# Optimization experiments

Hardware: AMD Instinct MI355X
Metric: run time of the kernel (lower is better)

Reference implementation:

```python
import jax, jax.numpy as jnp
import numpy as np

N = 100000
E_ADJ = 800000
E_RAY = 800000
IN_DIM = 2
HID = 64
HEADS = 2
NEG_SLOPE = 0.2  # PyG GATv2Conv default


def setup_inputs() -> dict:
    key = jax.random.key(0)
    ks = jax.random.split(key, 16)
    s = 0.1
    p = lambda k, shape: (jax.random.normal(k, shape, jnp.float32) * s)
    inp = {
        "x": jax.random.normal(ks[0], (N, IN_DIM), jnp.float32),
        "edge_adj": jax.random.randint(ks[1], (2, E_ADJ), 0, N, jnp.int32),
        "edge_ray": jax.random.randint(ks[2], (2, E_RAY), 0, N, jnp.int32),
        # layer 1 params, stacked over the 2 relation types [adjacent, ray]
        "l1_Wl": p(ks[3], (2, IN_DIM, HEADS * HID)),
        "l1_bl": jnp.zeros((2, HEADS * HID), jnp.float32),
        "l1_Wr": p(ks[4], (2, IN_DIM, HEADS * HID)),
        "l1_br": jnp.zeros((2, HEADS * HID), jnp.float32),
        "l1_att": p(ks[5], (2, HEADS, HID)),
        "l1_bias": jnp.zeros((2, HID), jnp.float32),
        # layer 2 params
        "l2_Wl": p(ks[6], (2, HID, HEADS * HID)),
        "l2_bl": jnp.zeros((2, HEADS * HID), jnp.float32),
        "l2_Wr": p(ks[7], (2, HID, HEADS * HID)),
        "l2_br": jnp.zeros((2, HEADS * HID), jnp.float32),
        "l2_att": p(ks[8], (2, HEADS, HID)),
        "l2_bias": jnp.zeros((2, HID), jnp.float32),
    }
    return inp


def _gatv2(x, src, dst, Wl, bl, Wr, br, att, bias):
    # GATv2Conv, concat=False, add_self_loops=False (PyG semantics)
    n = x.shape[0]
    H, C = att.shape
    xl = (x @ Wl + bl).reshape(n, H, C)  # source transform
    xr = (x @ Wr + br).reshape(n, H, C)  # target transform
    e = jax.nn.leaky_relu(xl[src] + xr[dst], NEG_SLOPE)  # [E,H,C]
    score = jnp.einsum('ehc,hc->eh', e, att)             # [E,H]
    # segment softmax over incoming edges per destination (per head)
    m = jax.ops.segment_max(score, dst, num_segments=n)  # only gathered at non-empty segs
    ex = jnp.exp(score - m[dst])
    denom = jax.ops.segment_sum(ex, dst, num_segments=n)
    alpha = ex / (denom[dst] + 1e-16)                    # [E,H]
    out = jax.ops.segment_sum(xl[src] * alpha[:, :, None], dst, num_segments=n)  # [N,H,C]
    return out.mean(axis=1) + bias                       # concat=False -> head mean


def _hetero_layer(x, ea, er, Wl, bl, Wr, br, att, bias):
    o_adj = _gatv2(x, ea[0], ea[1], Wl[0], bl[0], Wr[0], br[0], att[0], bias[0])
    o_ray = _gatv2(x, er[0], er[1], Wl[1], bl[1], Wr[1], br[1], att[1], bias[1])
    return 0.5 * (o_adj + o_ray)  # HeteroConv aggr='mean' over 2 relations


def reference(x, edge_adj, edge_ray,
              l1_Wl, l1_bl, l1_Wr, l1_br, l1_att, l1_bias,
              l2_Wl, l2_bl, l2_Wr, l2_br, l2_att, l2_bias):
    h = _hetero_layer(x, edge_adj, edge_ray, l1_Wl, l1_bl, l1_Wr, l1_br, l1_att, l1_bias)
    h = jax.nn.relu(h)
    out = _hetero_layer(h, edge_adj, edge_ray, l2_Wl, l2_bl, l2_Wr, l2_br, l2_att, l2_bias)
    return out
```

## Files before the change

kernel.cpp:

```cpp
#include <hip/hip_runtime.h>
#include <hip/hip_bf16.h>

typedef __hip_bfloat16 bf16;
typedef unsigned int uint;
typedef unsigned short ushort;
typedef __attribute__((ext_vector_type(8))) short short8;
typedef __attribute__((ext_vector_type(4))) float floatx4;

#define N_NODES 100000
#define N_PAD   100096
#define E_EDGES 800000
#define NBLK    98
#define EBLK    3125

static __device__ __forceinline__ uint packbf(float a, float b) {
  bf16 x = __float2bfloat16(a), y = __float2bfloat16(b);
  ushort ux = *reinterpret_cast<ushort*>(&x);
  ushort uy = *reinterpret_cast<ushort*>(&y);
  return (uint)ux | ((uint)uy << 16);
}
static __device__ __forceinline__ float lo16(uint u) { return __uint_as_float(u << 16); }
static __device__ __forceinline__ float hi16(uint u) { return __uint_as_float(u & 0xffff0000u); }

__global__ __launch_bounds__(256) void rank_k(
    const int* __restrict__ dst0, const int* __restrict__ dst1,
    int* fi0, int* fi1, int* __restrict__ rk0, int* __restrict__ rk1) {
  int i = blockIdx.x * 256 + threadIdx.x;
  int rel = blockIdx.y;
  const int* dst = rel ? dst1 : dst0;
  int* fi = rel ? fi1 : fi0;
  int* rk = rel ? rk1 : rk0;
  int d = dst[i];
  rk[i] = atomicAdd(&fi[d], 1);
}

__global__ __launch_bounds__(256) void scat_rank_k(
    const int* __restrict__ src0, const int* __restrict__ dst0,
    const int* __restrict__ src1, const int* __restrict__ dst1,
    const int* __restrict__ rk0, const int* __restrict__ rk1,
    const int* __restrict__ rp0, const int* __restrict__ rp1,
    int2* __restrict__ csd0, int2* __restrict__ csd1) {
  int i = blockIdx.x * 256 + threadIdx.x;
  int rel = blockIdx.y;
  const int* src = rel ? src1 : src0;
  const int* dst = rel ? dst1 : dst0;
  const int* rk = rel ? rk1 : rk0;
  const int* rp = rel ? rp1 : rp0;
  int2* csd = rel ? csd1 : csd0;
  int d = dst[i];
  int s = src[i];
  int pos = rp[d] + rk[i];
  csd[pos] = make_int2(s, d);
}

__global__ void scan_blk_k(const int* __restrict__ deg0, const int* __restrict__ deg1,
                           int* rp0, int* rp1, int* bsum) {
  __shared__ int s[1024];
  int r = blockIdx.y;
  const int* deg = r ? deg1 : deg0;
  int* rp = r ? rp1 : rp0;
  int i = blockIdx.x * 1024 + threadIdx.x;
  int v = (i < N_NODES) ? deg[i] : 0;
  s[threadIdx.x] = v;
  __syncthreads();
  for (int off = 1; off < 1024; off <<= 1) {
    int t = (threadIdx.x >= off) ? s[threadIdx.x - off] : 0;
    __syncthreads();
    s[threadIdx.x] += t;
    __syncthreads();
  }
  if (i < N_NODES) rp[i] = s[threadIdx.x] - v;
  if (threadIdx.x == 1023) bsum[r * NBLK + blockIdx.x] = s[1023];
}

__global__ void scan_top_k(int* bsum, int* rp0, int* rp1) {
  __shared__ int s[128];
  int r = blockIdx.x;
  int v = (threadIdx.x < NBLK) ? bsum[r * NBLK + threadIdx.x] : 0;
  s[threadIdx.x] = v;
  __syncthreads();
  for (int off = 1; off < 128; off <<= 1) {
    int t = (threadIdx.x >= off) ? s[threadIdx.x - off] : 0;
    __syncthreads();
    s[threadIdx.x] += t;
    __syncthreads();
  }
  if (threadIdx.x < NBLK) bsum[r * NBLK + threadIdx.x] = s[threadIdx.x] - v;
  if (threadIdx.x == 127) (r ? rp1 : rp0)[N_NODES] = s[127];
}

__global__ void scan_add_k(const int* __restrict__ bsum,
                           int* rp0, int* rp1, int* fi0, int* fi1) {
  int r = blockIdx.y;
  int i = blockIdx.x * 1024 + threadIdx.x;
  if (i >= N_NODES) return;
  int* rp = r ? rp1 : rp0;
  int* fi = r ? fi1 : fi0;
  int val = rp[i] + bsum[r * NBLK + blockIdx.x];
  rp[i] = val;
  fi[i] = val;
}

__global__ void wprep_k(const float* __restrict__ Wl, const float* __restrict__ Wr,
                        short* __restrict__ WT,
                        const float* __restrict__ l1Wl, const float* __restrict__ l1bl,
                        const float* __restrict__ l1Wr, const float* __restrict__ l1br,
                        const float* __restrict__ l1att, float* __restrict__ L1C) {
  if (blockIdx.x == 128) {
    int t = threadIdx.x;
    if (t < 20) {
      int rel = t / 10, rem = t % 10, h = rem / 5, v = rem % 5;
      const float* a = l1att + rel * 128 + h * 64;
      float sum = 0.f;
      for (int c = 0; c < 64; ++c) {
        int cc = h * 64 + c;
        float val;
        if (v == 0)      val = l1bl[rel * 128 + cc] + l1br[rel * 128 + cc];
        else if (v == 1) val = l1Wr[rel * 256 + cc];
        else if (v == 2) val = l1Wr[rel * 256 + 128 + cc];
        else if (v == 3) val = l1Wl[rel * 256 + cc];
        else             val = l1Wl[rel * 256 + 128 + cc];
        sum += a[c] * val;
      }
      L1C[t] = sum;
    }
    return;
  }
  int id2 = blockIdx.x * 256 + threadIdx.x;
  int rel = id2 >> 14;
  int id = id2 & 16383;
  int c = id >> 6, k = id & 63;
  const float* W = (c < 128) ? (Wl + rel * 8192) : (Wr + rel * 8192);
  int cc = c & 127;
  bf16 b = __float2bfloat16(W[k * 128 + cc]);
  WT[rel * 16384 + c * 64 + k] = *reinterpret_cast<short*>(&b);
}

__global__ __launch_bounds__(256) void l1score_k(
    const int2* __restrict__ csd0, const int2* __restrict__ csd1,
    const float* __restrict__ x,
    const float* __restrict__ Wl, const float* __restrict__ bl,
    const float* __restrict__ Wr, const float* __restrict__ br,
    const float* __restrict__ att, const float* __restrict__ l1c,
    float4* __restrict__ EX4) {
  __shared__ float sC[32 * 24];
  int rel = blockIdx.y;
  const int2* csd = rel ? csd1 : csd0;
  const float* Wl_r = Wl + rel * 256;
  const float* Wr_r = Wr + rel * 256;
  const float* bl_r = bl + rel * 128;
  const float* br_r = br + rel * 128;
  const float* att_r = att + rel * 128;
  int t = threadIdx.x;
  if (t < 128) {
    int c = t, ch = c >> 2, o = c & 3;
    sC[ch * 24 + 0 + o]  = bl_r[c] + br_r[c];
    sC[ch * 24 + 4 + o]  = Wr_r[c];
    sC[ch * 24 + 8 + o]  = Wr_r[128 + c];
    sC[ch * 24 + 12 + o] = Wl_r[c];
    sC[ch * 24 + 16 + o] = Wl_r[128 + c];
    sC[ch * 24 + 20 + o] = att_r[c];
  }
  const float* C = l1c + rel * 10;
  float q00 = C[0], qv00 = C[1], qv10 = C[2], qw00 = C[3], qw10 = C[4];
  float q01 = C[5], qv01 = C[6], qv11 = C[7], qw01 = C[8], qw11 = C[9];
  __syncthreads();
  int i = blockIdx.x * 256 + t;
  int2 sd = csd[i];
  int s = sd.x, d = sd.y;
  float2 xs = *(const float2*)(x + 2 * s);
  float2 xd = *(const float2*)(x + 2 * d);
  float t0a = 0.f, t0b = 0.f, t1a = 0.f, t1b = 0.f;
#pragma unroll
  for (int ch = 0; ch < 32; ++ch) {
    const float4* cp = (const float4*)(sC + ch * 24);
    float4 bb = cp[0], v0 = cp[1], v1 = cp[2], w0 = cp[3], w1 = cp[4], aa = cp[5];
    float e0 = bb.x + xd.x * v0.x + xd.y * v1.x + xs.x * w0.x + xs.y * w1.x;
    float e1 = bb.y + xd.x * v0.y + xd.y * v1.y + xs.x * w0.y + xs.y * w1.y;
    float e2 = bb.z + xd.x * v0.z + xd.y * v1.z + xs.x * w0.z + xs.y * w1.z;
    float e3 = bb.w + xd.x * v0.w + xd.y * v1.w + xs.x * w0.w + xs.y * w1.w;
    if (ch < 16) {
      t0a = fmaf(aa.x, fabsf(e0), t0a); t0b = fmaf(aa.y, fabsf(e1), t0b);
      t0a = fmaf(aa.z, fabsf(e2), t0a); t0b = fmaf(aa.w, fabsf(e3), t0b);
    } else {
      t1a = fmaf(aa.x, fabsf(e0), t1a); t1b = fmaf(aa.y, fabsf(e1), t1b);
      t1a = fmaf(aa.z, fabsf(e2), t1a); t1b = fmaf(aa.w, fabsf(e3), t1b);
    }
  }
  float T0 = t0a + t0b, T1 = t1a + t1b;
  float lin0 = q00 + xd.x * qv00 + xd.y * qv10 + xs.x * qw00 + xs.y * qw10;
  float lin1 = q01 + xd.x * qv01 + xd.y * qv11 + xs.x * qw01 + xs.y * qw11;
  float p0 = fmaf(0.4f, T0, 0.6f * lin0);
  float p1 = fmaf(0.4f, T1, 0.6f * lin1);
  EX4[(size_t)rel * E_EDGES + i] = make_float4(__expf(p0), __expf(p1), xs.x, xs.y);
}

__global__ __launch_bounds__(256) void l1agg_k(
    const int* __restrict__ rp0, const int* __restrict__ rp1,
    const float4* __restrict__ EX4, float* __restrict__ NA) {
  int g = (blockIdx.x * 256 + threadIdx.x) >> 2;
  int k = threadIdx.x & 3;
  if (g >= N_NODES) return;
  float p0 = 0.f, p1 = 0.f, p2 = 0.f, p3 = 0.f, p4 = 0.f, p5 = 0.f;
  float p6 = 0.f, p7 = 0.f, p8 = 0.f, p9 = 0.f, p10 = 0.f, p11 = 0.f;
  {
    int beg = rp0[g], end = rp0[g + 1];
    for (int j = beg + k; j < end; j += 4) {
      float4 e = EX4[j];
      p0 += e.x; p1 = fmaf(e.x, e.z, p1); p2 = fmaf(e.x, e.w, p2);
      p3 += e.y; p4 = fmaf(e.y, e.z, p4); p5 = fmaf(e.y, e.w, p5);
    }
  }
  {
    const float4* E1 = EX4 + E_EDGES;
    int beg = rp1[g], end = rp1[g + 1];
    for (int j = beg + k; j < end; j += 4) {
      float4 e = E1[j];
      p6 += e.x; p7 = fmaf(e.x, e.z, p7); p8 = fmaf(e.x, e.w, p8);
      p9 += e.y; p10 = fmaf(e.y, e.z, p10); p11 = fmaf(e.y, e.w, p11);
    }
  }
#define RED4(v) v += __shfl_xor(v, 1); v += __shfl_xor(v, 2);
  RED4(p0) RED4(p1) RED4(p2) RED4(p3) RED4(p4) RED4(p5)
  RED4(p6) RED4(p7) RED4(p8) RED4(p9) RED4(p10) RED4(p11)
#undef RED4
  float* na = NA + (size_t)g * 16;
  if (k == 0)      *(float4*)(na)     = make_float4(p0, p1, p2, p3);
  else if (k == 1) *(float4*)(na + 4) = make_float4(p4, p5, p6, p7);
  else if (k == 2) *(float4*)(na + 8) = make_float4(p8, p9, p10, p11);
}

__global__ __launch_bounds__(256) void l1finish_k(
    const float* __restrict__ NA,
    const float* __restrict__ Wl, const float* __restrict__ bl,
    const float* __restrict__ bias, uint2* __restrict__ HB2) {
  int idx = blockIdx.x * 256 + threadIdx.x;
  int d = idx >> 4, l = idx & 15;
  int c0 = 4 * l;
  const float* na = NA + (size_t)d * 16;
  float out0 = 0.f, out1 = 0.f, out2 = 0.f, out3 = 0.f;
#pragma unroll
  for (int r = 0; r < 2; ++r) {
    float a0c = 0.f, a1c = 0.f, a2c = 0.f, a3c = 0.f;
#pragma unroll
    for (int h = 0; h < 2; ++h) {
      float den = na[r * 6 + h * 3 + 0];
      float A0  = na[r * 6 + h * 3 + 1];
      float A1  = na[r * 6 + h * 3 + 2];
      float inv = 1.f / (den + 1e-16f);
      float a0 = A0 * inv, a1 = A1 * inv, S = den * inv;
      float4 W0 = *(const float4*)(Wl + r * 256 + h * 64 + c0);
      float4 W1 = *(const float4*)(Wl + r * 256 + 128 + h * 64 + c0);
      float4 B  = *(const float4*)(bl + r * 128 + h * 64 + c0);
      a0c += a0 * W0.x + a1 * W1.x + S * B.x;
      a1c += a0 * W0.y + a1 * W1.y + S * B.y;
      a2c += a0 * W0.z + a1 * W1.z + S * B.z;
      a3c += a0 * W0.w + a1 * W1.w + S * B.w;
    }
    float4 bi = *(const float4*)(bias + r * 64 + c0);
    out0 += 0.5f * a0c + bi.x;
    out1 += 0.5f * a1c + bi.y;
    out2 += 0.5f * a2c + bi.z;
    out3 += 0.5f * a3c + bi.w;
  }
  out0 = fmaxf(0.5f * out0, 0.f); out1 = fmaxf(0.5f * out1, 0.f);
  out2 = fmaxf(0.5f * out2, 0.f); out3 = fmaxf(0.5f * out3, 0.f);
  HB2[(size_t)d * 16 + l] = make_uint2(packbf(out0, out1), packbf(out2, out3));
}

__global__ __launch_bounds__(256) void mfma_t_k(const bf16* __restrict__ HB,
                                                const short* __restrict__ WTb,
                                                const float* __restrict__ blb,
                                                const float* __restrict__ brb,
                                                bf16* __restrict__ XL0,
                                                bf16* __restrict__ XR0,
                                                bf16* __restrict__ XL1,
                                                bf16* __restrict__ XR1) {
  __shared__ short sW[256 * 72];
  int rel = blockIdx.z;
  const short* WT = WTb + rel * 16384;
  const float* bl = blb + rel * 128;
  const float* br = brb + rel * 128;
  bf16* XLp = rel ? XL1 : XL0;
  bf16* XRp = rel ? XR1 : XR0;
  int t = threadIdx.x;
#pragma unroll
  for (int i = 0; i < 8; ++i) {
    int chunk = t + i * 256;
    int c = chunk >> 3, off = (chunk & 7) * 8;
    *(short8*)(&sW[c * 72 + off]) = *(const short8*)(WT + chunk * 8);
  }
  __syncthreads();
  int wave = t >> 6, lane = t & 63;
  int q = lane >> 4, m = lane & 15;
  int rowbase = blockIdx.x * 128 + wave * 32;
  short8 afr[2][2];
#pragma unroll
  for (int rt = 0; rt < 2; ++rt)
#pragma unroll
    for (int kh = 0; kh < 2; ++kh) {
      size_t row = (size_t)(rowbase + rt * 16 + m);
      afr[rt][kh] = *(const short8*)((const short*)HB + row * 64 + kh * 32 + q * 8);
    }
  for (int ct = 0; ct < 16; ++ct) {
    int col = ct * 16 + m;
    short8 b0 = *(const short8*)(&sW[col * 72 + q * 8]);
    short8 b1 = *(const short8*)(&sW[col * 72 + 32 + q * 8]);
    float bias = (col < 128) ? bl[col] : br[col - 128];
    bf16* X = (col < 128) ? XLp : XRp;
    int c128 = col & 127;
#pragma unroll
    for (int rt = 0; rt < 2; ++rt) {
      floatx4 acc = {0.f, 0.f, 0.f, 0.f};
      acc = __builtin_amdgcn_mfma_f32_16x16x32_bf16(afr[rt][0], b0, acc, 0, 0, 0);
      acc = __builtin_amdgcn_mfma_f32_16x16x32_bf16(afr[rt][1], b1, acc, 0, 0, 0);
      int r0 = rowbase + rt * 16 + q * 4;
#pragma unroll
      for (int i2 = 0; i2 < 4; ++i2) {
        int row = r0 + i2;
        if (row < N_NODES)
          X[(size_t)row * 128 + c128] = __float2bfloat16(acc[i2] + bias);
      }
    }
  }
}

struct EdgeAcc { float a0, a1, a2, a3, den; };

static __device__ __forceinline__ void edge_step(
    uint2 u, float xr0, float xr1, float xr2, float xr3,
    float at0, float at1, float at2, float at3, EdgeAcc& A) {
  float x0 = lo16(u.x), x1 = hi16(u.x), x2 = lo16(u.y), x3 = hi16(u.y);
  float e0 = x0 + xr0; e0 = e0 > 0.f ? e0 : 0.2f * e0;
  float e1 = x1 + xr1; e1 = e1 > 0.f ? e1 : 0.2f * e1;
  float e2 = x2 + xr2; e2 = e2 > 0.f ? e2 : 0.2f * e2;
  float e3 = x3 + xr3; e3 = e3 > 0.f ? e3 : 0.2f * e3;
  float p = e0 * at0 + e1 * at1 + e2 * at2 + e3 * at3;
  p += __shfl_xor(p, 1);
  p += __shfl_xor(p, 2);
  p += __shfl_xor(p, 4);
  p += __shfl_xor(p, 8);
  float ex = __expf(p);
  A.den += ex;
  A.a0 += ex * x0; A.a1 += ex * x1; A.a2 += ex * x2; A.a3 += ex * x3;
}

__global__ __launch_bounds__(256) void aggf_k(
    const int* __restrict__ rp0, const int2* __restrict__ csd0,
    const int* __restrict__ rp1, const int2* __restrict__ csd1,
    const bf16* __restrict__ XL0, const bf16* __restrict__ XR0,
    const bf16* __restrict__ XL1, const bf16* __restrict__ XR1,
    const float* __restrict__ att,
    const float* __restrict__ bias,
    float* __restrict__ outf) {
  int d = (blockIdx.x * 256 + threadIdx.x) >> 6;
  int lane = threadIdx.x & 63;
  if (d >= N_NODES) return;
  int half = lane >> 5;
  int l = lane & 31;
  int beg0 = rp0[d], end0 = rp0[d + 1];
  int beg1 = rp1[d], end1 = rp1[d + 1];
  const float* at = att + 4 * l;
  const float* bt = att + 128 + 4 * l;
  float at0 = at[0], at1 = at[1], at2 = at[2], at3 = at[3];
  float bt0 = bt[0], bt1 = bt[1], bt2 = bt[2], bt3 = bt[3];
  uint2 ur0 = *(const uint2*)(XR0 + (size_t)d * 128 + 4 * l);
  uint2 ur1 = *(const uint2*)(XR1 + (size_t)d * 128 + 4 * l);
  float xa0 = lo16(ur0.x), xa1 = hi16(ur0.x), xa2 = lo16(ur0.y), xa3 = hi16(ur0.y);
  float xb0 = lo16(ur1.x), xb1 = hi16(ur1.x), xb2 = lo16(ur1.y), xb3 = hi16(ur1.y);
  EdgeAcc A = {0.f, 0.f, 0.f, 0.f, 0.f};
  EdgeAcc B = {0.f, 0.f, 0.f, 0.f, 0.f};
  {
    int j = beg0 + half;
    for (; j + 2 < end0; j += 4) {
      int sA = csd0[j].x, sB = csd0[j + 2].x;
      uint2 uA = *(const uint2*)(XL0 + (size_t)sA * 128 + 4 * l);
      uint2 uB = *(const uint2*)(XL0 + (size_t)sB * 128 + 4 * l);
      edge_step(uA, xa0, xa1, xa2, xa3, at0, at1, at2, at3, A);
      edge_step(uB, xa0, xa1, xa2, xa3, at0, at1, at2, at3, A);
    }
    for (; j < end0; j += 2) {
      int s = csd0[j].x;
      uint2 u = *(const uint2*)(XL0 + (size_t)s * 128 + 4 * l);
      edge_step(u, xa0, xa1, xa2, xa3, at0, at1, at2, at3, A);
    }
  }
  {
    int j = beg1 + half;
    for (; j + 2 < end1; j += 4) {
      int sA = csd1[j].x, sB = csd1[j + 2].x;
      uint2 uA = *(const uint2*)(XL1 + (size_t)sA * 128 + 4 * l);
      uint2 uB = *(const uint2*)(XL1 + (size_t)sB * 128 + 4 * l);
      edge_step(uA, xb0, xb1, xb2, xb3, bt0, bt1, bt2, bt3, B);
      edge_step(uB, xb0, xb1, xb2, xb3, bt0, bt1, bt2, bt3, B);
    }
    for (; j < end1; j += 2) {
      int s = csd1[j].x;
      uint2 u = *(const uint2*)(XL1 + (size_t)s * 128 + 4 * l);
      edge_step(u, xb0, xb1, xb2, xb3, bt0, bt1, bt2, bt3, B);
    }
  }
#define C32(v) v += __shfl_xor(v, 32);
  C32(A.den) C32(A.a0) C32(A.a1) C32(A.a2) C32(A.a3)
  C32(B.den) C32(B.a0) C32(B.a1) C32(B.a2) C32(B.a3)
#undef C32
  float invA = 1.f / (A.den + 1e-16f);
  float invB = 1.f / (B.den + 1e-16f);
  A.a0 *= invA; A.a1 *= invA; A.a2 *= invA; A.a3 *= invA;
  B.a0 *= invB; B.a1 *= invB; B.a2 *= invB; B.a3 *= invB;
  float t0 = 0.5f * (A.a0 + __shfl_xor(A.a0, 16));
  float t1 = 0.5f * (A.a1 + __shfl_xor(A.a1, 16));
  float t2 = 0.5f * (A.a2 + __shfl_xor(A.a2, 16));
  float t3 = 0.5f * (A.a3 + __shfl_xor(A.a3, 16));
  float u0 = 0.5f * (B.a0 + __shfl_xor(B.a0, 16));
  float u1 = 0.5f * (B.a1 + __shfl_xor(B.a1, 16));
  float u2 = 0.5f * (B.a2 + __shfl_xor(B.a2, 16));
  float u3 = 0.5f * (B.a3 + __shfl_xor(B.a3, 16));
  if (lane >= 16) return;
  int c0 = 4 * lane;
  t0 += bias[c0]; t1 += bias[c0 + 1]; t2 += bias[c0 + 2]; t3 += bias[c0 + 3];
  u0 += bias[64 + c0]; u1 += bias[64 + c0 + 1];
  u2 += bias[64 + c0 + 2]; u3 += bias[64 + c0 + 3];
  float v0 = 0.5f * (t0 + u0);
  float v1 = 0.5f * (t1 + u1);
  float v2 = 0.5f * (t2 + u2);
  float v3 = 0.5f * (t3 + u3);
  *(float4*)(outf + (size_t)d * 64 + c0) = make_float4(v0, v1, v2, v3);
}

extern "C" void kernel_launch(void* const* d_in, const int* in_sizes, int n_in,
                              void* d_out, int out_size, void* d_ws, size_t ws_size,
                              hipStream_t stream) {
  const float* x       = (const float*)d_in[0];
  const int*   e_adj   = (const int*)d_in[1];
  const int*   e_ray   = (const int*)d_in[2];
  const float* l1_Wl   = (const float*)d_in[3];
  const float* l1_bl   = (const float*)d_in[4];
  const float* l1_Wr   = (const float*)d_in[5];
  const float* l1_br   = (const float*)d_in[6];
  const float* l1_att  = (const float*)d_in[7];
  const float* l1_bias = (const float*)d_in[8];
  const float* l2_Wl   = (const float*)d_in[9];
  const float* l2_bl   = (const float*)d_in[10];
  const float* l2_Wr   = (const float*)d_in[11];
  const float* l2_br   = (const float*)d_in[12];
  const float* l2_att  = (const float*)d_in[13];
  const float* l2_bias = (const float*)d_in[14];
  float* out = (float*)d_out;

  char* w = (char*)d_ws;
  size_t off = 0;
  auto alloc = [&](size_t bytes) -> char* {
    char* p = w + off;
    off += (bytes + 255) & ~(size_t)255;
    return p;
  };
  bf16* XL0  = (bf16*)alloc((size_t)N_PAD * 128 * 2);
  bf16* XR0  = (bf16*)alloc((size_t)N_PAD * 128 * 2);
  bf16* XL1  = (bf16*)alloc((size_t)N_PAD * 128 * 2);
  bf16* XR1  = (bf16*)alloc((size_t)N_PAD * 128 * 2);
  bf16* HB   = (bf16*)alloc((size_t)N_PAD * 64 * 2);
  short* WT  = (short*)alloc(2 * 16384 * 2);
  int* RP0   = (int*)alloc((size_t)(N_NODES + 1) * 4);
  int* RP1   = (int*)alloc((size_t)(N_NODES + 1) * 4);
  int* FI0   = (int*)alloc((size_t)N_NODES * 4);
  int* FI1   = (int*)alloc((size_t)N_NODES * 4);
  int2* CSD0 = (int2*)alloc((size_t)E_EDGES * 8);
  int2* CSD1 = (int2*)alloc((size_t)E_EDGES * 8);
  int* BSUM  = (int*)alloc(2 * NBLK * 4);
  float* L1C = (float*)alloc(20 * 4);

  float4* EX4 = (float4*)XL0;
  float* NA   = (float*)((char*)XL0 + 25600000);
  int* RK0    = (int*)XL1;
  int* RK1    = (int*)((char*)XL1 + 3200000);

  const int* src_adj = e_adj;
  const int* dst_adj = e_adj + E_EDGES;
  const int* src_ray = e_ray;
  const int* dst_ray = e_ray + E_EDGES;

  const int WNB = (N_NODES * 64) / 256;
  const int MB  = N_PAD / 128;

  size_t fispan = (size_t)((char*)FI1 - (char*)FI0) + (size_t)N_NODES * 4;
  hipMemsetAsync(FI0, 0, fispan, stream);
  rank_k<<<dim3(EBLK, 2), 256, 0, stream>>>(dst_adj, dst_ray, FI0, FI1, RK0, RK1);
  scan_blk_k<<<dim3(NBLK, 2), 1024, 0, stream>>>(FI0, FI1, RP0, RP1, BSUM);
  scan_top_k<<<2, 128, 0, stream>>>(BSUM, RP0, RP1);
  scan_add_k<<<dim3(NBLK, 2), 1024, 0, stream>>>(BSUM, RP0, RP1, FI0, FI1);
  scat_rank_k<<<dim3(EBLK, 2), 256, 0, stream>>>(src_adj, dst_adj, src_ray, dst_ray,
                                                 RK0, RK1, RP0, RP1, CSD0, CSD1);
  wprep_k<<<129, 256, 0, stream>>>(l2_Wl, l2_Wr, WT,
                                   l1_Wl, l1_bl, l1_Wr, l1_br, l1_att, L1C);

  l1score_k<<<dim3(EBLK, 2), 256, 0, stream>>>(
      CSD0, CSD1, x, l1_Wl, l1_bl, l1_Wr, l1_br, l1_att, L1C, EX4);
  l1agg_k<<<(N_NODES * 4 + 255) / 256, 256, 0, stream>>>(RP0, RP1, EX4, NA);
  l1finish_k<<<(N_NODES * 16) / 256, 256, 0, stream>>>(NA, l1_Wl, l1_bl, l1_bias,
                                                       (uint2*)HB);

  mfma_t_k<<<dim3(MB, 1, 2), 256, 0, stream>>>(HB, WT, l2_bl, l2_br,
                                               XL0, XR0, XL1, XR1);
  aggf_k<<<WNB, 256, 0, stream>>>(RP0, CSD0, RP1, CSD1, XL0, XR0, XL1, XR1,
                                  l2_att, l2_bias, out);
}
```

Before: 423.3 us.

## Widen layer-2 edge gathers to 16-byte loads and precompute layer-1 coefficient table

The final aggregation kernel now splits each wavefront into four groups of 16 lanes. Each lane loads 8 bf16 features with one 16-byte load instead of 4 with an 8-byte load, so four edges are processed in parallel per wave instead of two, and the per-edge shuffle reduction drops one step. The layer-1 score kernel no longer rebuilds its coefficient table in shared memory with a block barrier. It reads a table that the weight-prep kernel writes once to global memory. The trade-offs are more registers per lane and more cross-group reduction shuffles at the end. The score kernel's table reads now go through the global/constant cache instead of LDS.

```diff
diff --git a/kernel.cpp b/kernel.cpp
--- a/kernel.cpp
+++ b/kernel.cpp
@@ -105,9 +105,21 @@
                         short* __restrict__ WT,
                         const float* __restrict__ l1Wl, const float* __restrict__ l1bl,
                         const float* __restrict__ l1Wr, const float* __restrict__ l1br,
-                        const float* __restrict__ l1att, float* __restrict__ L1C) {
+                        const float* __restrict__ l1att, float* __restrict__ L1C,
+                        float* __restrict__ SCG) {
   if (blockIdx.x == 128) {
     int t = threadIdx.x;
+    {
+      int rel = t >> 7, c = t & 127;
+      int ch = c >> 2, o = c & 3;
+      float* g = SCG + rel * 768 + ch * 24;
+      g[0 + o]  = l1bl[rel * 128 + c] + l1br[rel * 128 + c];
+      g[4 + o]  = l1Wr[rel * 256 + c];
+      g[8 + o]  = l1Wr[rel * 256 + 128 + c];
+      g[12 + o] = l1Wl[rel * 256 + c];
+      g[16 + o] = l1Wl[rel * 256 + 128 + c];
+      g[20 + o] = l1att[rel * 128 + c];
+    }
     if (t < 20) {
       int rel = t / 10, rem = t % 10, h = rem / 5, v = rem % 5;
       const float* a = l1att + rel * 128 + h * 64;
@@ -139,33 +151,15 @@
 __global__ __launch_bounds__(256) void l1score_k(
     const int2* __restrict__ csd0, const int2* __restrict__ csd1,
     const float* __restrict__ x,
-    const float* __restrict__ Wl, const float* __restrict__ bl,
-    const float* __restrict__ Wr, const float* __restrict__ br,
-    const float* __restrict__ att, const float* __restrict__ l1c,
+    const float* __restrict__ scg, const float* __restrict__ l1c,
     float4* __restrict__ EX4) {
-  __shared__ float sC[32 * 24];
   int rel = blockIdx.y;
   const int2* csd = rel ? csd1 : csd0;
-  const float* Wl_r = Wl + rel * 256;
-  const float* Wr_r = Wr + rel * 256;
-  const float* bl_r = bl + rel * 128;
-  const float* br_r = br + rel * 128;
-  const float* att_r = att + rel * 128;
-  int t = threadIdx.x;
-  if (t < 128) {
-    int c = t, ch = c >> 2, o = c & 3;
-    sC[ch * 24 + 0 + o]  = bl_r[c] + br_r[c];
-    sC[ch * 24 + 4 + o]  = Wr_r[c];
-    sC[ch * 24 + 8 + o]  = Wr_r[128 + c];
-    sC[ch * 24 + 12 + o] = Wl_r[c];
-    sC[ch * 24 + 16 + o] = Wl_r[128 + c];
-    sC[ch * 24 + 20 + o] = att_r[c];
-  }
+  const float* sC = scg + rel * 768;
   const float* C = l1c + rel * 10;
   float q00 = C[0], qv00 = C[1], qv10 = C[2], qw00 = C[3], qw10 = C[4];
   float q01 = C[5], qv01 = C[6], qv11 = C[7], qw01 = C[8], qw11 = C[9];
-  __syncthreads();
-  int i = blockIdx.x * 256 + t;
+  int i = blockIdx.x * 256 + threadIdx.x;
   int2 sd = csd[i];
   int s = sd.x, d = sd.y;
   float2 xs = *(const float2*)(x + 2 * s);
@@ -325,24 +319,28 @@
   }
 }
 
-struct EdgeAcc { float a0, a1, a2, a3, den; };
-
-static __device__ __forceinline__ void edge_step(
-    uint2 u, float xr0, float xr1, float xr2, float xr3,
-    float at0, float at1, float at2, float at3, EdgeAcc& A) {
-  float x0 = lo16(u.x), x1 = hi16(u.x), x2 = lo16(u.y), x3 = hi16(u.y);
-  float e0 = x0 + xr0; e0 = e0 > 0.f ? e0 : 0.2f * e0;
-  float e1 = x1 + xr1; e1 = e1 > 0.f ? e1 : 0.2f * e1;
-  float e2 = x2 + xr2; e2 = e2 > 0.f ? e2 : 0.2f * e2;
-  float e3 = x3 + xr3; e3 = e3 > 0.f ? e3 : 0.2f * e3;
-  float p = e0 * at0 + e1 * at1 + e2 * at2 + e3 * at3;
+static __device__ __forceinline__ void edge_step16(
+    uint4 u, const float (&xr)[8], const float (&at)[8],
+    float (&a)[8], float& den) {
+  float x[8];
+  x[0] = lo16(u.x); x[1] = hi16(u.x);
+  x[2] = lo16(u.y); x[3] = hi16(u.y);
+  x[4] = lo16(u.z); x[5] = hi16(u.z);
+  x[6] = lo16(u.w); x[7] = hi16(u.w);
+  float p = 0.f;
+#pragma unroll
+  for (int j = 0; j < 8; ++j) {
+    float e = x[j] + xr[j];
+    float le = fmaxf(e, 0.2f * e);
+    p = fmaf(at[j], le, p);
+  }
   p += __shfl_xor(p, 1);
   p += __shfl_xor(p, 2);
   p += __shfl_xor(p, 4);
-  p += __shfl_xor(p, 8);
   float ex = __expf(p);
-  A.den += ex;
-  A.a0 += ex * x0; A.a1 += ex * x1; A.a2 += ex * x2; A.a3 += ex * x3;
+  den += ex;
+#pragma unroll
+  for (int j = 0; j < 8; ++j) a[j] = fmaf(ex, x[j], a[j]);
 }
 
 __global__ __launch_bounds__(256) void aggf_k(
@@ -356,76 +354,99 @@
   int d = (blockIdx.x * 256 + threadIdx.x) >> 6;
   int lane = threadIdx.x & 63;
   if (d >= N_NODES) return;
-  int half = lane >> 5;
-  int l = lane & 31;
+  int g = lane >> 4;
+  int k = lane & 15;
   int beg0 = rp0[d], end0 = rp0[d + 1];
   int beg1 = rp1[d], end1 = rp1[d + 1];
-  const float* at = att + 4 * l;
-  const float* bt = att + 128 + 4 * l;
-  float at0 = at[0], at1 = at[1], at2 = at[2], at3 = at[3];
-  float bt0 = bt[0], bt1 = bt[1], bt2 = bt[2], bt3 = bt[3];
-  uint2 ur0 = *(const uint2*)(XR0 + (size_t)d * 128 + 4 * l);
-  uint2 ur1 = *(const uint2*)(XR1 + (size_t)d * 128 + 4 * l);
-  float xa0 = lo16(ur0.x), xa1 = hi16(ur0.x), xa2 = lo16(ur0.y), xa3 = hi16(ur0.y);
-  float xb0 = lo16(ur1.x), xb1 = hi16(ur1.x), xb2 = lo16(ur1.y), xb3 = hi16(ur1.y);
-  EdgeAcc A = {0.f, 0.f, 0.f, 0.f, 0.f};
-  EdgeAcc B = {0.f, 0.f, 0.f, 0.f, 0.f};
+  float at0[8], at1[8], xr0v[8], xr1v[8];
   {
-    int j = beg0 + half;
-    for (; j + 2 < end0; j += 4) {
-      int sA = csd0[j].x, sB = csd0[j + 2].x;
-      uint2 uA = *(const uint2*)(XL0 + (size_t)sA * 128 + 4 * l);
-      uint2 uB = *(const uint2*)(XL0 + (size_t)sB * 128 + 4 * l);
-      edge_step(uA, xa0, xa1, xa2, xa3, at0, at1, at2, at3, A);
-      edge_step(uB, xa0, xa1, xa2, xa3, at0, at1, at2, at3, A);
-    }
-    for (; j < end0; j += 2) {
+    float4 a0 = *(const float4*)(att + 8 * k);
+    float4 a1 = *(const float4*)(att + 8 * k + 4);
+    at0[0] = a0.x; at0[1] = a0.y; at0[2] = a0.z; at0[3] = a0.w;
+    at0[4] = a1.x; at0[5] = a1.y; at0[6] = a1.z; at0[7] = a1.w;
+    float4 b0 = *(const float4*)(att + 128 + 8 * k);
+    float4 b1 = *(const float4*)(att + 128 + 8 * k + 4);
+    at1[0] = b0.x; at1[1] = b0.y; at1[2] = b0.z; at1[3] = b0.w;
+    at1[4] = b1.x; at1[5] = b1.y; at1[6] = b1.z; at1[7] = b1.w;
+    uint4 uA = *(const uint4*)((const char*)XR0 + (size_t)d * 256 + k * 16);
+    xr0v[0] = lo16(uA.x); xr0v[1] = hi16(uA.x);
+    xr0v[2] = lo16(uA.y); xr0v[3] = hi16(uA.y);
+    xr0v[4] = lo16(uA.z); xr0v[5] = hi16(uA.z);
+    xr0v[6] = lo16(uA.w); xr0v[7] = hi16(uA.w);
+    uint4 uB = *(const uint4*)((const char*)XR1 + (size_t)d * 256 + k * 16);
+    xr1v[0] = lo16(uB.x); xr1v[1] = hi16(uB.x);
+    xr1v[2] = lo16(uB.y); xr1v[3] = hi16(uB.y);
+    xr1v[4] = lo16(uB.z); xr1v[5] = hi16(uB.z);
+    xr1v[6] = lo16(uB.w); xr1v[7] = hi16(uB.w);
+  }
+  float aA[8] = {0.f, 0.f, 0.f, 0.f, 0.f, 0.f, 0.f, 0.f};
+  float aB[8] = {0.f, 0.f, 0.f, 0.f, 0.f, 0.f, 0.f, 0.f};
+  float denA = 0.f, denB = 0.f;
+  {
+    int j = beg0 + g;
+    for (; j + 4 < end0; j += 8) {
+      int sA = csd0[j].x, sB = csd0[j + 4].x;
+      uint4 uA = *(const uint4*)((const char*)XL0 + (size_t)sA * 256 + k * 16);
+      uint4 uB = *(const uint4*)((const char*)XL0 + (size_t)sB * 256 + k * 16);
+      edge_step16(uA, xr0v, at0, aA, denA);
+      edge_step16(uB, xr0v, at0, aA, denA);
+    }
+    for (; j < end0; j += 4) {
       int s = csd0[j].x;
-      uint2 u = *(const uint2*)(XL0 + (size_t)s * 128 + 4 * l);
-      edge_step(u, xa0, xa1, xa2, xa3, at0, at1, at2, at3, A);
+      uint4 u = *(const uint4*)((const char*)XL0 + (size_t)s * 256 + k * 16);
+      edge_step16(u, xr0v, at0, aA, denA);
     }
   }
   {
-    int j = beg1 + half;
-    for (; j + 2 < end1; j += 4) {
-      int sA = csd1[j].x, sB = csd1[j + 2].x;
-      uint2 uA = *(const uint2*)(XL1 + (size_t)sA * 128 + 4 * l);
-      uint2 uB = *(const uint2*)(XL1 + (size_t)sB * 128 + 4 * l);
-      edge_step(uA, xb0, xb1, xb2, xb3, bt0, bt1, bt2, bt3, B);
-      edge_step(uB, xb0, xb1, xb2, xb3, bt0, bt1, bt2, bt3, B);
-    }
-    for (; j < end1; j += 2) {
+    int j = beg1 + g;
+    for (; j + 4 < end1; j += 8) {
+      int sA = csd1[j].x, sB = csd1[j + 4].x;
+      uint4 uA = *(const uint4*)((const char*)XL1 + (size_t)sA * 256 + k * 16);
+      uint4 uB = *(const uint4*)((const char*)XL1 + (size_t)sB * 256 + k * 16);
+      edge_step16(uA, xr1v, at1, aB, denB);
+      edge_step16(uB, xr1v, at1, aB, denB);
+    }
+    for (; j < end1; j += 4) {
       int s = csd1[j].x;
-      uint2 u = *(const uint2*)(XL1 + (size_t)s * 128 + 4 * l);
-      edge_step(u, xb0, xb1, xb2, xb3, bt0, bt1, bt2, bt3, B);
-    }
-  }
-#define C32(v) v += __shfl_xor(v, 32);
-  C32(A.den) C32(A.a0) C32(A.a1) C32(A.a2) C32(A.a3)
-  C32(B.den) C32(B.a0) C32(B.a1) C32(B.a2) C32(B.a3)
-#undef C32
-  float invA = 1.f / (A.den + 1e-16f);
-  float invB = 1.f / (B.den + 1e-16f);
-  A.a0 *= invA; A.a1 *= invA; A.a2 *= invA; A.a3 *= invA;
-  B.a0 *= invB; B.a1 *= invB; B.a2 *= invB; B.a3 *= invB;
-  float t0 = 0.5f * (A.a0 + __shfl_xor(A.a0, 16));
-  float t1 = 0.5f * (A.a1 + __shfl_xor(A.a1, 16));
-  float t2 = 0.5f * (A.a2 + __shfl_xor(A.a2, 16));
-  float t3 = 0.5f * (A.a3 + __shfl_xor(A.a3, 16));
-  float u0 = 0.5f * (B.a0 + __shfl_xor(B.a0, 16));
-  float u1 = 0.5f * (B.a1 + __shfl_xor(B.a1, 16));
-  float u2 = 0.5f * (B.a2 + __shfl_xor(B.a2, 16));
-  float u3 = 0.5f * (B.a3 + __shfl_xor(B.a3, 16));
-  if (lane >= 16) return;
-  int c0 = 4 * lane;
-  t0 += bias[c0]; t1 += bias[c0 + 1]; t2 += bias[c0 + 2]; t3 += bias[c0 + 3];
-  u0 += bias[64 + c0]; u1 += bias[64 + c0 + 1];
-  u2 += bias[64 + c0 + 2]; u3 += bias[64 + c0 + 3];
-  float v0 = 0.5f * (t0 + u0);
-  float v1 = 0.5f * (t1 + u1);
-  float v2 = 0.5f * (t2 + u2);
-  float v3 = 0.5f * (t3 + u3);
-  *(float4*)(outf + (size_t)d * 64 + c0) = make_float4(v0, v1, v2, v3);
+      uint4 u = *(const uint4*)((const char*)XL1 + (size_t)s * 256 + k * 16);
+      edge_step16(u, xr1v, at1, aB, denB);
+    }
+  }
+#pragma unroll
+  for (int j = 0; j < 8; ++j) {
+    aA[j] += __shfl_xor(aA[j], 16); aA[j] += __shfl_xor(aA[j], 32);
+    aB[j] += __shfl_xor(aB[j], 16); aB[j] += __shfl_xor(aB[j], 32);
+  }
+  denA += __shfl_xor(denA, 16); denA += __shfl_xor(denA, 32);
+  denB += __shfl_xor(denB, 16); denB += __shfl_xor(denB, 32);
+  float invA = 1.f / (denA + 1e-16f);
+  float invB = 1.f / (denB + 1e-16f);
+  float tA[8], tB[8];
+#pragma unroll
+  for (int j = 0; j < 8; ++j) {
+    float ta = aA[j] * invA;
+    tA[j] = 0.5f * (ta + __shfl_xor(ta, 8));
+    float tb = aB[j] * invB;
+    tB[j] = 0.5f * (tb + __shfl_xor(tb, 8));
+  }
+  if (lane >= 8) return;
+  int c0 = 8 * k;
+  float4 b0a = *(const float4*)(bias + c0);
+  float4 b0b = *(const float4*)(bias + c0 + 4);
+  float4 b1a = *(const float4*)(bias + 64 + c0);
+  float4 b1b = *(const float4*)(bias + 64 + c0 + 4);
+  float o[8];
+  o[0] = 0.5f * ((tA[0] + b0a.x) + (tB[0] + b1a.x));
+  o[1] = 0.5f * ((tA[1] + b0a.y) + (tB[1] + b1a.y));
+  o[2] = 0.5f * ((tA[2] + b0a.z) + (tB[2] + b1a.z));
+  o[3] = 0.5f * ((tA[3] + b0a.w) + (tB[3] + b1a.w));
+  o[4] = 0.5f * ((tA[4] + b0b.x) + (tB[4] + b1b.x));
+  o[5] = 0.5f * ((tA[5] + b0b.y) + (tB[5] + b1b.y));
+  o[6] = 0.5f * ((tA[6] + b0b.z) + (tB[6] + b1b.z));
+  o[7] = 0.5f * ((tA[7] + b0b.w) + (tB[7] + b1b.w));
+  float* op = outf + (size_t)d * 64 + c0;
+  *(float4*)(op)     = make_float4(o[0], o[1], o[2], o[3]);
+  *(float4*)(op + 4) = make_float4(o[4], o[5], o[6], o[7]);
 }
 
 extern "C" void kernel_launch(void* const* d_in, const int* in_sizes, int n_in,
@@ -469,6 +490,7 @@
   int2* CSD1 = (int2*)alloc((size_t)E_EDGES * 8);
   int* BSUM  = (int*)alloc(2 * NBLK * 4);
   float* L1C = (float*)alloc(20 * 4);
+  float* SCG = (float*)alloc(2 * 768 * 4);
 
   float4* EX4 = (float4*)XL0;
   float* NA   = (float*)((char*)XL0 + 25600000);
@@ -492,10 +514,9 @@
   scat_rank_k<<<dim3(EBLK, 2), 256, 0, stream>>>(src_adj, dst_adj, src_ray, dst_ray,
                                                  RK0, RK1, RP0, RP1, CSD0, CSD1);
   wprep_k<<<129, 256, 0, stream>>>(l2_Wl, l2_Wr, WT,
-                                   l1_Wl, l1_bl, l1_Wr, l1_br, l1_att, L1C);
-
-  l1score_k<<<dim3(EBLK, 2), 256, 0, stream>>>(
-      CSD0, CSD1, x, l1_Wl, l1_bl, l1_Wr, l1_br, l1_att, L1C, EX4);
+                                   l1_Wl, l1_bl, l1_Wr, l1_br, l1_att, L1C, SCG);
+
+  l1score_k<<<dim3(EBLK, 2), 256, 0, stream>>>(CSD0, CSD1, x, SCG, L1C, EX4);
   l1agg_k<<<(N_NODES * 4 + 255) / 256, 256, 0, stream>>>(RP0, RP1, EX4, NA);
   l1finish_k<<<(N_NODES * 16) / 256, 256, 0, stream>>>(NA, l1_Wl, l1_bl, l1_bias,
                                                        (uint2*)HB);
```

New measurement: 441.4 us. 4.3% more time.
